# Performance work log

Measured on AMD Instinct MI355X. Metric: run time of the kernel, lower is better.

## Reference

```python
import jax, jax.numpy as jnp
import numpy as np

B, T, N, DIN, DR, DH, K = 8, 40, 1024, 16, 64, 64, 3
DT = 0.05
N_EULER = 2  # Euler sub-steps per observation interval (time_points per step)


def dconv(A, x, W, b):
    feats = [x]
    h = x
    for _ in range(K - 1):
        h = jnp.einsum('bnm,bmd->bnd', A, h)
        feats.append(h)
    return jnp.concatenate(feats, -1) @ W + b


def dcgru(x, h, A, Wg, bg, Wc, bc):
    g = jax.nn.sigmoid(dconv(A, jnp.concatenate([x, h], -1), Wg, bg))
    r, u = jnp.split(g, 2, -1)
    c = jnp.tanh(dconv(A, jnp.concatenate([x, r * h], -1), Wc, bc))
    return u * h + (1.0 - u) * c


def ode_f(h, A, W0, b0, Wout, bout):
    return jnp.tanh(jnp.tanh(dconv(A, h, W0, b0)) @ Wout + bout)


def setup_inputs() -> dict:
    key = jax.random.key(0)
    ks = jax.random.split(key, 32)
    p = lambda k, s: 0.1 * jax.random.normal(k, s, dtype=jnp.float32)
    values = jax.random.normal(ks[0], (B, T, N, DIN), dtype=jnp.float32)
    masks = (jax.random.uniform(ks[1], (B, T, N, DIN)) > 0.3).astype(jnp.float32)
    u = jax.random.uniform(ks[2], (B, N, N), dtype=jnp.float32)
    A = u / u.sum(-1, keepdims=True)  # row-normalized dense diffusion matrix
    d = dict(values=values, masks=masks, A=A,
             h0=p(ks[3], (1, 1, DR)) * 0.1, z0=p(ks[4], (1, 1, DR)) * 0.1,
             gV_Wg=p(ks[5], ((DIN + DR) * K, 2 * DR)), gV_bg=jnp.zeros((2 * DR,)),
             gV_Wc=p(ks[6], ((DIN + DR) * K, DR)), gV_bc=jnp.zeros((DR,)),
             gG_Wg=p(ks[7], ((DIN + DR) * K, 2 * DR)), gG_bg=jnp.zeros((2 * DR,)),
             gG_Wc=p(ks[8], ((DIN + DR) * K, DR)), gG_bc=jnp.zeros((DR,)),
             oV_W0=p(ks[9], (DR * K, DH)), oV_b0=jnp.zeros((DH,)),
             oV_Wout=p(ks[10], (DH, DR)), oV_bout=jnp.zeros((DR,)),
             oG_W0=p(ks[11], (DR * K, DH)), oG_b0=jnp.zeros((DH,)),
             oG_Wout=p(ks[12], (DH, DR)), oG_bout=jnp.zeros((DR,)),
             Wz1=p(ks[13], (DR, DR)), bz1=jnp.zeros((DR,)),
             Wz2=p(ks[14], (DR, DR)), bz2=jnp.zeros((DR,)),
             Wz3=p(ks[15], (DR, DR)), bz3=jnp.zeros((DR,)),
             Wo=p(ks[16], (DR, DIN)), bo=jnp.zeros((DIN,)))
    return d


def reference(values, masks, A, h0, z0,
              gV_Wg, gV_bg, gV_Wc, gV_bc, gG_Wg, gG_bg, gG_Wc, gG_bc,
              oV_W0, oV_b0, oV_Wout, oV_bout, oG_W0, oG_b0, oG_Wout, oG_bout,
              Wz1, bz1, Wz2, bz2, Wz3, bz3, Wo, bo):
    X = values * masks  # [B,T,N,DIN]
    obs = (jnp.abs(masks).sum(-1, keepdims=True) > 1e-4).astype(values.dtype)  # [B,T,N,1]
    hv = jnp.broadcast_to(h0, (B, N, DR))
    zv = jnp.broadcast_to(z0, (B, N, DR))
    dt = DT / N_EULER

    def step(carry, inp):
        hv, zv = carry
        x, m = inp  # [B,N,DIN], [B,N,1]
        for _ in range(N_EULER):  # Euler ODE integration over the interval
            hv = hv + dt * ode_f(hv, A, oV_W0, oV_b0, oV_Wout, oV_bout)
            zv = zv + dt * ode_f(zv, A, oG_W0, oG_b0, oG_Wout, oG_bout)
        hv1, zv1 = hv, zv
        hv2 = dcgru(x, hv1, A, gV_Wg, gV_bg, gV_Wc, gV_bc)
        zv2 = dcgru(x, zv1, A, gG_Wg, gG_bg, gG_Wc, gG_bc)
        hv_new = hv1 * (1.0 - m) + hv2 * m
        zv_new = zv1 * (1.0 - m) + zv2 * m
        return (hv_new, zv_new), (hv1, zv1, hv_new)

    xs = (jnp.swapaxes(X, 0, 1), jnp.swapaxes(obs, 0, 1))  # time-major
    _, (hv_pre, zv_pre, hv_post) = jax.lax.scan(step, (hv, zv), xs)
    hv_pre = jnp.swapaxes(hv_pre, 0, 1)   # [B,T,N,DR]
    zv_pre = jnp.swapaxes(zv_pre, 0, 1)
    gate = jax.nn.sigmoid(jnp.tanh(jnp.tanh(zv_pre @ Wz1 + bz1) @ Wz2 + bz2) @ Wz3 + bz3)
    X_pred = (hv_pre * gate) @ Wo + bo
    return X_pred[:, 1:, :, :]
```

## Files before the change

### kernel.cpp

```cpp
#include <hip/hip_runtime.h>
#include <math.h>


#define T_ 40

typedef __attribute__((ext_vector_type(8))) short short8;
typedef __attribute__((ext_vector_type(4))) float f32x4;

__device__ __forceinline__ float sigm(float x) { return 1.0f / (1.0f + expf(-x)); }

__device__ __forceinline__ unsigned short bfrnd(float x) {
  union { float f; unsigned int u; } v; v.f = x;
  unsigned int u = v.u + 0x7fffu + ((v.u >> 16) & 1u);
  return (unsigned short)(u >> 16);
}
__device__ __forceinline__ unsigned int pk2(float a, float b) {
  return (unsigned int)bfrnd(a) | ((unsigned int)bfrnd(b) << 16);
}

__global__ __launch_bounds__(256) void k_init(float* __restrict__ S, unsigned short* __restrict__ SB,
                                              const float* __restrict__ h0,
                                              const float* __restrict__ z0) {
  int idx = blockIdx.x * 256 + threadIdx.x;
  int c = idx & 63;
  S[idx] = (idx < (8192 * 64)) ? h0[c] : z0[c];
  int cc = (idx >> 10) & 63;
  float v2 = ((idx >> 16) < 8) ? h0[cc] : z0[cc];
  SB[idx] = bfrnd(v2);
}

__global__ __launch_bounds__(256) void k_asA(const float* __restrict__ A, unsigned short* __restrict__ AS) {
  size_t j = ((size_t)blockIdx.x * 256 + threadIdx.x) * 8;
  if (j >= (size_t)8 * 1024 * 1024) return;
  int b = (int)(j >> 20);
  size_t rem = j & 1048575;
  int r = (int)(rem >> 10), k = (int)(rem & 1023);
  const float* src = A + ((size_t)b << 20) + (size_t)r * 1024 + k;
  float4 v0 = *(const float4*)src;
  float4 v1 = *(const float4*)(src + 4);
  uint4 o;
  o.x = pk2(v0.x, v0.y); o.y = pk2(v0.z, v0.w);
  o.z = pk2(v1.x, v1.y); o.w = pk2(v1.z, v1.w);
  *(uint4*)(AS + ((size_t)b * 2048 + r) * 1024 + k) = o;
}

__global__ __launch_bounds__(256) void k_xb(const float* __restrict__ values,
                                            const float* __restrict__ masks,
                                            unsigned short* __restrict__ XB) {
  const int bt = blockIdx.x;
  const int n0 = blockIdx.y * 256;
  __shared__ float Ls[256][17];
  const int tid = threadIdx.x;
  size_t base = ((size_t)bt * 1024 + n0 + tid) * 16;
#pragma unroll
  for (int c4 = 0; c4 < 4; ++c4) {
    float4 v = *(const float4*)&values[base + c4 * 4];
    float4 m = *(const float4*)&masks[base + c4 * 4];
    Ls[tid][c4 * 4 + 0] = v.x * m.x; Ls[tid][c4 * 4 + 1] = v.y * m.y;
    Ls[tid][c4 * 4 + 2] = v.z * m.z; Ls[tid][c4 * 4 + 3] = v.w * m.w;
  }
  __syncthreads();
  const int c = tid >> 4, seg = tid & 15;
  uint4 o1, o2;
  o1.x = pk2(Ls[seg * 16 + 0][c], Ls[seg * 16 + 1][c]);
  o1.y = pk2(Ls[seg * 16 + 2][c], Ls[seg * 16 + 3][c]);
  o1.z = pk2(Ls[seg * 16 + 4][c], Ls[seg * 16 + 5][c]);
  o1.w = pk2(Ls[seg * 16 + 6][c], Ls[seg * 16 + 7][c]);
  o2.x = pk2(Ls[seg * 16 + 8][c], Ls[seg * 16 + 9][c]);
  o2.y = pk2(Ls[seg * 16 + 10][c], Ls[seg * 16 + 11][c]);
  o2.z = pk2(Ls[seg * 16 + 12][c], Ls[seg * 16 + 13][c]);
  o2.w = pk2(Ls[seg * 16 + 14][c], Ls[seg * 16 + 15][c]);
  unsigned short* dst = XB + ((size_t)bt * 16 + c) * 1024 + n0 + seg * 16;
  *(uint4*)dst = o1;
  *(uint4*)(dst + 8) = o2;
}

__global__ __launch_bounds__(256) void k_a2(const float* __restrict__ A, unsigned short* __restrict__ AS) {
  const int b = blockIdx.z;
  const int m0 = blockIdx.y * 128, n0 = blockIdx.x * 128;
  const float* Ab = A + ((size_t)b << 20);
  __shared__ float As[8][136];
  __shared__ float Bs[8][136];
  const int tx = threadIdx.x & 15, ty = threadIdx.x >> 4;
  float acc[8][8];
#pragma unroll
  for (int m = 0; m < 8; ++m)
#pragma unroll
    for (int n = 0; n < 8; ++n) acc[m][n] = 0.0f;

  for (int k0 = 0; k0 < 1024; k0 += 8) {
    int mm = threadIdx.x >> 1, k4 = (threadIdx.x & 1) * 4;
    float4 va = *(const float4*)&Ab[(size_t)(m0 + mm) * 1024 + k0 + k4];
    As[k4 + 0][mm] = va.x; As[k4 + 1][mm] = va.y; As[k4 + 2][mm] = va.z; As[k4 + 3][mm] = va.w;
    int kk = threadIdx.x >> 5, nn = (threadIdx.x & 31) * 4;
    float4 vb = *(const float4*)&Ab[(size_t)(k0 + kk) * 1024 + n0 + nn];
    *(float4*)&Bs[kk][nn] = vb;
    __syncthreads();
#pragma unroll
    for (int k = 0; k < 8; ++k) {
      float a[8], bb[8];
      *(float4*)&a[0] = *(float4*)&As[k][ty * 8];
      *(float4*)&a[4] = *(float4*)&As[k][ty * 8 + 4];
      *(float4*)&bb[0] = *(float4*)&Bs[k][tx * 8];
      *(float4*)&bb[4] = *(float4*)&Bs[k][tx * 8 + 4];
#pragma unroll
      for (int m = 0; m < 8; ++m)
#pragma unroll
        for (int n = 0; n < 8; ++n) acc[m][n] += a[m] * bb[n];
    }
    __syncthreads();
  }
#pragma unroll
  for (int m = 0; m < 8; ++m) {
    unsigned short* C = AS + ((size_t)b * 2048 + 1024 + m0 + ty * 8 + m) * 1024 + n0 + tx * 8;
    uint4 o;
    o.x = pk2(acc[m][0], acc[m][1]); o.y = pk2(acc[m][2], acc[m][3]);
    o.z = pk2(acc[m][4], acc[m][5]); o.w = pk2(acc[m][6], acc[m][7]);
    *(uint4*)C = o;
  }
}

template <int MODE>
__global__ __launch_bounds__(256) void k_fused(
    const unsigned short* __restrict__ AS,
    const unsigned short* __restrict__ XB,
    const unsigned short* __restrict__ SBr,
    unsigned short* __restrict__ SBw,
    const unsigned short* __restrict__ RHBin,
    unsigned short* __restrict__ RHBout,
    float* __restrict__ S, float* __restrict__ RH, float* __restrict__ U,
    const float* __restrict__ values, const float* __restrict__ masks,
    const float* __restrict__ W1h, const float* __restrict__ b1h,
    const float* __restrict__ W2h, const float* __restrict__ b2h,
    const float* __restrict__ W1z, const float* __restrict__ b1z,
    const float* __restrict__ W2z, const float* __restrict__ b2z,
    int t) {
  constexpr int NT = (MODE == 0) ? 8 : 9;
  constexpr int KF = (MODE == 0) ? 192 : 240;
  constexpr int FW = KF + 1;
  constexpr int NTILE = 2 + NT;
  constexpr int CHK = (MODE == 0) ? 64 : 48;
  constexpr int CW = (MODE == 1) ? 128 : 64;
  constexpr int CWP = CW + 4;
  constexpr int NCHK = KF / CHK;
  constexpr int R0_STAGE = 2 * NTILE * 1024;
  constexpr int R0_W = CHK * CWP * 4 + ((MODE == 0) ? 16 * 68 * 4 : 0);
  constexpr int R0 = (R0_STAGE > R0_W) ? R0_STAGE : R0_W;

  __shared__ __align__(16) char r0[R0];
  __shared__ float feats[2][16][FW];
  __shared__ float Ts[2][64][17];
  __shared__ float Ms[16];

  unsigned short* stg = (unsigned short*)r0;
  float* Wcs = (float*)r0;
  float* T1 = (float*)(r0 + 64 * 68 * 4);

  const int tid = threadIdx.x;
  const int w = tid >> 6, l = tid & 63;
  const int lr = l & 15, lk = l >> 4;
  const int b = blockIdx.y;
  const int n0 = blockIdx.x * 16;

  const unsigned short* ag =
      AS + ((size_t)b * 2048 + (w == 1 ? 1024 : 0) + n0 + lr) * 1024 + lk * 8;

  auto tsrc = [&](int ct) -> const unsigned short* {
    if (MODE == 0) {
      int st = ct >> 2, cl = ct & 3;
      return SBr + ((size_t)(st * 8 + b) * 64 + cl * 16 + lr) * 1024 + lk * 8;
    } else {
      if (ct == 0) return XB + ((size_t)(b * T_ + t) * 16 + lr) * 1024 + lk * 8;
      const unsigned short* base = (MODE == 1) ? SBr : RHBin;
      int st = (ct <= 4) ? 0 : 1;
      int cl = (ct <= 4) ? (ct - 1) : (ct - 5);
      return base + ((size_t)(st * 8 + b) * 64 + cl * 16 + lr) * 1024 + lk * 8;
    }
  };
  const unsigned short* bs0 = tsrc(w);
  const unsigned short* bs1 = tsrc(w + 4);
  const unsigned short* bs2 = (NT == 9 && w == 0) ? tsrc(8) : bs0;
  const int bcnt = (NT == 9 && w == 0) ? 3 : 2;

  if (MODE == 0) {
    for (int idx = tid; idx < 512; idx += 256) {
      int st = idx >> 8, rr = (idx >> 4) & 15, c4 = idx & 15;
      float4 v = *(const float4*)&S[((size_t)(st * 8 + b) * 1024 + n0 + rr) * 64 + c4 * 4];
      feats[st][rr][c4 * 4 + 0] = v.x; feats[st][rr][c4 * 4 + 1] = v.y;
      feats[st][rr][c4 * 4 + 2] = v.z; feats[st][rr][c4 * 4 + 3] = v.w;
    }
  } else {
    for (int idx = tid; idx < 64; idx += 256) {
      int rr = idx >> 2, c4 = idx & 3;
      size_t xo = ((size_t)(b * T_ + t) * 1024 + n0 + rr) * 16 + c4 * 4;
      float4 v = *(const float4*)&values[xo];
      float4 m = *(const float4*)&masks[xo];
      float xv[4] = {v.x * m.x, v.y * m.y, v.z * m.z, v.w * m.w};
#pragma unroll
      for (int j = 0; j < 4; ++j) {
        feats[0][rr][c4 * 4 + j] = xv[j];
        feats[1][rr][c4 * 4 + j] = xv[j];
      }
    }
    const float* bp = (MODE == 1) ? S : RH;
    for (int idx = tid; idx < 512; idx += 256) {
      int st = idx >> 8, rr = (idx >> 4) & 15, c4 = idx & 15;
      float4 v = *(const float4*)&bp[((size_t)(st * 8 + b) * 1024 + n0 + rr) * 64 + c4 * 4];
      feats[st][rr][16 + c4 * 4 + 0] = v.x; feats[st][rr][16 + c4 * 4 + 1] = v.y;
      feats[st][rr][16 + c4 * 4 + 2] = v.z; feats[st][rr][16 + c4 * 4 + 3] = v.w;
    }
  }
  if (MODE == 2 && tid < 16) {
    int n = n0 + tid;
    size_t xo = ((size_t)(b * T_ + t) * 1024 + n) * 16;
    float s = 0.0f;
    for (int d = 0; d < 16; ++d) s += fabsf(masks[xo + d]);
    Ms[tid] = (s > 1e-4f) ? 1.0f : 0.0f;
  }

  f32x4 acc[2][3];
#pragma unroll
  for (int rt = 0; rt < 2; ++rt)
#pragma unroll
    for (int ci = 0; ci < 3; ++ci) acc[rt][ci] = (f32x4){0.f, 0.f, 0.f, 0.f};

#define GLD(SRC, SLOT, BUF)                                                                   \
  __builtin_amdgcn_global_load_lds(                                                           \
      (const __attribute__((address_space(1))) void*)(SRC),                                   \
      (__attribute__((address_space(3))) void*)(stg + ((BUF)*NTILE + (SLOT)) * 512), 16, 0, 0)

#define STAGE(BUF, K0)                                                                        \
  {                                                                                           \
    if (w < 2) GLD(ag + (K0), w, BUF);                                                        \
    GLD(bs0 + (K0), 2 + w, BUF);                                                              \
    GLD(bs1 + (K0), 2 + w + 4, BUF);                                                          \
    if (NT == 9 && w == 0) GLD(bs2 + (K0), 2 + 8, BUF);                                       \
  }

  int cur = 0;
  STAGE(0, 0)
  __syncthreads();
  for (int step = 0; step < 32; ++step) {
    const int nxt = cur ^ 1;
    if (step < 31) STAGE(nxt, (step + 1) * 32)
    short8 a0f = *(const short8*)&stg[(cur * NTILE + 0) * 512 + l * 8];
    short8 a1f = *(const short8*)&stg[(cur * NTILE + 1) * 512 + l * 8];
    short8 b0f = *(const short8*)&stg[(cur * NTILE + 2 + w) * 512 + l * 8];
    short8 b1f = *(const short8*)&stg[(cur * NTILE + 2 + w + 4) * 512 + l * 8];
    acc[0][0] = __builtin_amdgcn_mfma_f32_16x16x32_bf16(a0f, b0f, acc[0][0], 0, 0, 0);
    acc[1][0] = __builtin_amdgcn_mfma_f32_16x16x32_bf16(a1f, b0f, acc[1][0], 0, 0, 0);
    acc[0][1] = __builtin_amdgcn_mfma_f32_16x16x32_bf16(a0f, b1f, acc[0][1], 0, 0, 0);
    acc[1][1] = __builtin_amdgcn_mfma_f32_16x16x32_bf16(a1f, b1f, acc[1][1], 0, 0, 0);
    if (NT == 9 && w == 0) {
      short8 b2f = *(const short8*)&stg[(cur * NTILE + 2 + 8) * 512 + l * 8];
      acc[0][2] = __builtin_amdgcn_mfma_f32_16x16x32_bf16(a0f, b2f, acc[0][2], 0, 0, 0);
      acc[1][2] = __builtin_amdgcn_mfma_f32_16x16x32_bf16(a1f, b2f, acc[1][2], 0, 0, 0);
    }
    __syncthreads();
    cur = nxt;
  }
#undef STAGE
#undef GLD

#pragma unroll
  for (int ci = 0; ci < 3; ++ci) {
    if (ci < bcnt) {
      const int ct = w + ci * 4;
#pragma unroll
      for (int rt = 0; rt < 2; ++rt) {
#pragma unroll
        for (int j = 0; j < 4; ++j) {
          float v = acc[rt][ci][j];
          int row = lk * 4 + j;
          if (MODE == 0) {
            int st = ct >> 2;
            feats[st][row][64 + rt * 64 + (ct & 3) * 16 + lr] = v;
          } else {
            if (ct == 0) {
              int col = 80 + rt * 80 + lr;
              feats[0][row][col] = v;
              feats[1][row][col] = v;
            } else {
              int st = (ct <= 4) ? 0 : 1;
              int cl = (ct <= 4) ? (ct - 1) : (ct - 5);
              feats[st][row][80 + rt * 80 + 16 + cl * 16 + lr] = v;
            }
          }
        }
      }
    }
  }
  __syncthreads();

  const int r_ = tid >> 4, cq = tid & 15;

  if (MODE == 0) {
    for (int st = 0; st < 2; ++st) {
      const float* W1 = st ? W1z : W1h;
      const float* B1 = st ? b1z : b1h;
      const float* W2 = st ? W2z : W2h;
      const float* B2 = st ? b2z : b2h;
      float a4[4] = {0, 0, 0, 0};
      for (int kc = 0; kc < NCHK; ++kc) {
        __syncthreads();
        for (int idx = tid; idx < 1024; idx += 256) {
          int k = idx >> 4, c4 = idx & 15;
          *(float4*)&Wcs[k * 68 + c4 * 4] = *(const float4*)&W1[(size_t)(kc * 64 + k) * 64 + c4 * 4];
        }
        __syncthreads();
#pragma unroll 8
        for (int k = 0; k < 64; ++k) {
          float f = feats[st][r_][kc * 64 + k];
          float4 w4 = *(float4*)&Wcs[k * 68 + cq * 4];
          a4[0] += f * w4.x; a4[1] += f * w4.y; a4[2] += f * w4.z; a4[3] += f * w4.w;
        }
      }
#pragma unroll
      for (int j = 0; j < 4; ++j) T1[r_ * 68 + cq * 4 + j] = tanhf(a4[j] + B1[cq * 4 + j]);
      __syncthreads();
      for (int idx = tid; idx < 1024; idx += 256) {
        int k = idx >> 4, c4 = idx & 15;
        *(float4*)&Wcs[k * 68 + c4 * 4] = *(const float4*)&W2[(size_t)k * 64 + c4 * 4];
      }
      __syncthreads();
      float o4[4] = {0, 0, 0, 0};
#pragma unroll 8
      for (int k = 0; k < 64; ++k) {
        float f = T1[r_ * 68 + k];
        float4 w4 = *(float4*)&Wcs[k * 68 + cq * 4];
        o4[0] += f * w4.x; o4[1] += f * w4.y; o4[2] += f * w4.z; o4[3] += f * w4.w;
      }
      size_t g = ((size_t)(st * 8 + b) * 1024 + n0 + r_) * 64 + cq * 4;
#pragma unroll
      for (int j = 0; j < 4; ++j) {
        float ns = S[g + j] + 0.025f * tanhf(o4[j] + B2[cq * 4 + j]);
        S[g + j] = ns;
        Ts[st][cq * 4 + j][r_] = ns;
      }
      __syncthreads();
    }
  } else if (MODE == 1) {
    for (int st = 0; st < 2; ++st) {
      const float* W1 = st ? W1z : W1h;
      const float* B1 = st ? b1z : b1h;
      float a8[8] = {0, 0, 0, 0, 0, 0, 0, 0};
      for (int kc = 0; kc < NCHK; ++kc) {
        __syncthreads();
        for (int idx = tid; idx < 1536; idx += 256) {
          int k = idx >> 5, c4 = idx & 31;
          *(float4*)&Wcs[k * 132 + c4 * 4] = *(const float4*)&W1[(size_t)(kc * 48 + k) * 128 + c4 * 4];
        }
        __syncthreads();
#pragma unroll 8
        for (int k = 0; k < 48; ++k) {
          float f = feats[st][r_][kc * 48 + k];
          float4 wA = *(float4*)&Wcs[k * 132 + cq * 8];
          float4 wB = *(float4*)&Wcs[k * 132 + cq * 8 + 4];
          a8[0] += f * wA.x; a8[1] += f * wA.y; a8[2] += f * wA.z; a8[3] += f * wA.w;
          a8[4] += f * wB.x; a8[5] += f * wB.y; a8[6] += f * wB.z; a8[7] += f * wB.w;
        }
      }
      size_t g = ((size_t)(st * 8 + b) * 1024 + n0 + r_) * 64;
      if (cq < 8) {
#pragma unroll
        for (int j = 0; j < 8; ++j) {
          int c = cq * 8 + j;
          float rr = sigm(a8[j] + B1[c]);
          float rhv = rr * feats[st][r_][16 + c];
          RH[g + c] = rhv;
          Ts[st][c][r_] = rhv;
        }
      } else {
#pragma unroll
        for (int j = 0; j < 8; ++j) {
          int c = (cq - 8) * 8 + j;
          U[g + c] = sigm(a8[j] + B1[64 + c]);
        }
      }
      __syncthreads();
    }
  } else {
    for (int st = 0; st < 2; ++st) {
      const float* W1 = st ? W1z : W1h;
      const float* B1 = st ? b1z : b1h;
      float a4[4] = {0, 0, 0, 0};
      for (int kc = 0; kc < NCHK; ++kc) {
        __syncthreads();
        for (int idx = tid; idx < 768; idx += 256) {
          int k = idx >> 4, c4 = idx & 15;
          *(float4*)&Wcs[k * 68 + c4 * 4] = *(const float4*)&W1[(size_t)(kc * 48 + k) * 64 + c4 * 4];
        }
        __syncthreads();
#pragma unroll 8
        for (int k = 0; k < 48; ++k) {
          float f = feats[st][r_][kc * 48 + k];
          float4 w4 = *(float4*)&Wcs[k * 68 + cq * 4];
          a4[0] += f * w4.x; a4[1] += f * w4.y; a4[2] += f * w4.z; a4[3] += f * w4.w;
        }
      }
      size_t g = ((size_t)(st * 8 + b) * 1024 + n0 + r_) * 64;
      float m = Ms[r_];
#pragma unroll
      for (int j = 0; j < 4; ++j) {
        int c = cq * 4 + j;
        float cc = tanhf(a4[j] + B1[c]);
        float h1 = S[g + c];
        float u = U[g + c];
        float h2 = u * h1 + (1.0f - u) * cc;
        float ns = h1 * (1.0f - m) + h2 * m;
        S[g + c] = ns;
        Ts[st][c][r_] = ns;
      }
      __syncthreads();
    }
  }

  {
    unsigned short* dstbuf = (MODE == 1) ? RHBout : SBw;
    int st = tid >> 7, c = (tid >> 1) & 63, p = tid & 1;
    float* tp = &Ts[st][c][p * 8];
    uint4 o;
    o.x = pk2(tp[0], tp[1]); o.y = pk2(tp[2], tp[3]);
    o.z = pk2(tp[4], tp[5]); o.w = pk2(tp[6], tp[7]);
    *(uint4*)(dstbuf + ((size_t)(st * 8 + b) * 64 + c) * 1024 + n0 + p * 8) = o;
  }
}

__global__ __launch_bounds__(256) void k_out(const float* __restrict__ S,
    const float* __restrict__ Wz1, const float* __restrict__ bz1,
    const float* __restrict__ Wz2, const float* __restrict__ bz2,
    const float* __restrict__ Wz3, const float* __restrict__ bz3,
    const float* __restrict__ Wo, const float* __restrict__ bo,
    float* __restrict__ out, int t) {
  __shared__ float Zs[32][68];
  __shared__ float T1s[32][68];
  __shared__ float Hs[32][68];
  __shared__ float Wc[64][64];
  __shared__ float bias[64];
  const int rowbase = blockIdx.x * 32;
  const int r = threadIdx.x >> 3, q = threadIdx.x & 7;

  for (int idx = threadIdx.x; idx < 2048; idx += 256) {
    int rr = idx >> 6, c = idx & 63;
    size_t g = (size_t)(rowbase + rr);
    Zs[rr][c] = S[(size_t)524288 + g * 64 + c];
    Hs[rr][c] = S[g * 64 + c];
  }

#define LAYER(SRC, DST, WPTR, BPTR, ACT)                                            \
  __syncthreads();                                                                  \
  for (int idx = threadIdx.x; idx < 1024; idx += 256)                               \
    ((float4*)Wc)[idx] = ((const float4*)(WPTR))[idx];                              \
  if (threadIdx.x < 64) bias[threadIdx.x] = (BPTR)[threadIdx.x];                    \
  __syncthreads();                                                                  \
  {                                                                                 \
    float ac[8] = {0, 0, 0, 0, 0, 0, 0, 0};                                         \
    _Pragma("unroll 8") for (int k = 0; k < 64; ++k) {                              \
      float f = SRC[r][k];                                                          \
      float4 w0 = *(float4*)&Wc[k][q * 8];                                          \
      float4 w1 = *(float4*)&Wc[k][q * 8 + 4];                                      \
      ac[0] += f * w0.x; ac[1] += f * w0.y; ac[2] += f * w0.z; ac[3] += f * w0.w;   \
      ac[4] += f * w1.x; ac[5] += f * w1.y; ac[6] += f * w1.z; ac[7] += f * w1.w;   \
    }                                                                               \
    _Pragma("unroll") for (int j = 0; j < 8; ++j)                                   \
        DST[r][q * 8 + j] = ACT(ac[j] + bias[q * 8 + j]);                           \
  }

  LAYER(Zs, T1s, Wz1, bz1, tanhf)
  LAYER(T1s, Zs, Wz2, bz2, tanhf)
  LAYER(Zs, T1s, Wz3, bz3, sigm)
#undef LAYER

  __syncthreads();
  for (int idx = threadIdx.x; idx < 256; idx += 256)
    ((float4*)Wc)[idx] = ((const float4*)Wo)[idx];
  if (threadIdx.x < 16) bias[threadIdx.x] = bo[threadIdx.x];
  __syncthreads();

  const float* WcF = &Wc[0][0];
  float a0 = 0.0f, a1 = 0.0f;
#pragma unroll 8
  for (int k = 0; k < 64; ++k) {
    float f = Hs[r][k] * T1s[r][k];
    a0 += f * WcF[k * 16 + q * 2];
    a1 += f * WcF[k * 16 + q * 2 + 1];
  }
  size_t g = (size_t)(rowbase + r);
  int b = (int)(g >> 10), n = (int)(g & 1023);
  size_t o = (((size_t)b * 39 + (t - 1)) * 1024 + n) * 16 + q * 2;
  out[o]     = a0 + bias[q * 2];
  out[o + 1] = a1 + bias[q * 2 + 1];
}

extern "C" void kernel_launch(void* const* d_in, const int* in_sizes, int n_in,
                              void* d_out, int out_size, void* d_ws, size_t ws_size,
                              hipStream_t stream) {
  const float* values = (const float*)d_in[0];
  const float* masks  = (const float*)d_in[1];
  const float* A      = (const float*)d_in[2];
  const float* h0     = (const float*)d_in[3];
  const float* z0     = (const float*)d_in[4];
  const float* gV_Wg  = (const float*)d_in[5];
  const float* gV_bg  = (const float*)d_in[6];
  const float* gV_Wc  = (const float*)d_in[7];
  const float* gV_bc  = (const float*)d_in[8];
  const float* gG_Wg  = (const float*)d_in[9];
  const float* gG_bg  = (const float*)d_in[10];
  const float* gG_Wc  = (const float*)d_in[11];
  const float* gG_bc  = (const float*)d_in[12];
  const float* oV_W0  = (const float*)d_in[13];
  const float* oV_b0  = (const float*)d_in[14];
  const float* oV_Wout = (const float*)d_in[15];
  const float* oV_bout = (const float*)d_in[16];
  const float* oG_W0  = (const float*)d_in[17];
  const float* oG_b0  = (const float*)d_in[18];
  const float* oG_Wout = (const float*)d_in[19];
  const float* oG_bout = (const float*)d_in[20];
  const float* Wz1 = (const float*)d_in[21];
  const float* bz1 = (const float*)d_in[22];
  const float* Wz2 = (const float*)d_in[23];
  const float* bz2 = (const float*)d_in[24];
  const float* Wz3 = (const float*)d_in[25];
  const float* bz3 = (const float*)d_in[26];
  const float* Wo  = (const float*)d_in[27];
  const float* bo  = (const float*)d_in[28];
  float* out = (float*)d_out;

  if (ws_size < (size_t)62914560) return;
  char* ws = (char*)d_ws;
  float* S            = (float*)(ws + 0);
  float* RH           = (float*)(ws + 4194304);
  float* U            = (float*)(ws + 8388608);
  unsigned short* SBa = (unsigned short*)(ws + 12582912);
  unsigned short* SBb = (unsigned short*)(ws + 14680064);
  unsigned short* RHB = (unsigned short*)(ws + 16777216);
  unsigned short* XB  = (unsigned short*)(ws + 18874368);
  unsigned short* AS  = (unsigned short*)(ws + 29360128);

  k_asA<<<4096, 256, 0, stream>>>(A, AS);
  k_a2<<<dim3(8, 8, 8), 256, 0, stream>>>(A, AS);
  k_init<<<4096, 256, 0, stream>>>(S, SBa, h0, z0);
  k_xb<<<dim3(320, 4), 256, 0, stream>>>(values, masks, XB);

  const dim3 fg(64, 8);
  for (int t = 0; t < T_; ++t) {
    k_fused<0><<<fg, 256, 0, stream>>>(AS, XB, SBa, SBb, RHB, RHB, S, RH, U, values, masks,
                                       oV_W0, oV_b0, oV_Wout, oV_bout,
                                       oG_W0, oG_b0, oG_Wout, oG_bout, t);
    k_fused<0><<<fg, 256, 0, stream>>>(AS, XB, SBb, SBa, RHB, RHB, S, RH, U, values, masks,
                                       oV_W0, oV_b0, oV_Wout, oV_bout,
                                       oG_W0, oG_b0, oG_Wout, oG_bout, t);
    if (t >= 1)
      k_out<<<256, 256, 0, stream>>>(S, Wz1, bz1, Wz2, bz2, Wz3, bz3, Wo, bo, out, t);
    if (t < T_ - 1) {
      k_fused<1><<<fg, 256, 0, stream>>>(AS, XB, SBa, SBb, RHB, RHB, S, RH, U, values, masks,
                                         gV_Wg, gV_bg, nullptr, nullptr,
                                         gG_Wg, gG_bg, nullptr, nullptr, t);
      k_fused<2><<<fg, 256, 0, stream>>>(AS, XB, SBa, SBa, RHB, RHB, S, RH, U, values, masks,
                                         gV_Wc, gV_bc, nullptr, nullptr,
                                         gG_Wc, gG_bc, nullptr, nullptr, t);
    }
  }
}
```

Before: 8.997 ms.

## Fuse output head into ODE kernel, MFMA A^2 precompute, remap block grid

```diff
diff --git a/kernel.cpp b/kernel.cpp
--- a/kernel.cpp
+++ b/kernel.cpp
@@ -42,6 +42,84 @@
   o.x = pk2(v0.x, v0.y); o.y = pk2(v0.z, v0.w);
   o.z = pk2(v1.x, v1.y); o.w = pk2(v1.z, v1.w);
   *(uint4*)(AS + ((size_t)b * 2048 + r) * 1024 + k) = o;
+}
+
+__global__ __launch_bounds__(256) void k_tr(const float* __restrict__ A, unsigned short* __restrict__ ATB) {
+  const int b = blockIdx.z, k0 = blockIdx.y * 64, n0 = blockIdx.x * 64;
+  __shared__ float Ls[64][65];
+  const float* Ab = A + ((size_t)b << 20);
+  for (int idx = threadIdx.x; idx < 1024; idx += 256) {
+    int kr = idx >> 4, cg = idx & 15;
+    float4 v = *(const float4*)&Ab[(size_t)(k0 + kr) * 1024 + n0 + cg * 4];
+    Ls[kr][cg * 4 + 0] = v.x; Ls[kr][cg * 4 + 1] = v.y;
+    Ls[kr][cg * 4 + 2] = v.z; Ls[kr][cg * 4 + 3] = v.w;
+  }
+  __syncthreads();
+  const int nr = threadIdx.x >> 2, seg = threadIdx.x & 3;
+  const int ks = seg * 16;
+  uint4 o1, o2;
+  o1.x = pk2(Ls[ks + 0][nr], Ls[ks + 1][nr]);
+  o1.y = pk2(Ls[ks + 2][nr], Ls[ks + 3][nr]);
+  o1.z = pk2(Ls[ks + 4][nr], Ls[ks + 5][nr]);
+  o1.w = pk2(Ls[ks + 6][nr], Ls[ks + 7][nr]);
+  o2.x = pk2(Ls[ks + 8][nr], Ls[ks + 9][nr]);
+  o2.y = pk2(Ls[ks + 10][nr], Ls[ks + 11][nr]);
+  o2.z = pk2(Ls[ks + 12][nr], Ls[ks + 13][nr]);
+  o2.w = pk2(Ls[ks + 14][nr], Ls[ks + 15][nr]);
+  unsigned short* dst = ATB + ((size_t)b * 1024 + n0 + nr) * 1024 + k0 + ks;
+  *(uint4*)dst = o1;
+  *(uint4*)(dst + 8) = o2;
+}
+
+__global__ __launch_bounds__(256) void k_a2m(unsigned short* __restrict__ AS,
+                                             const unsigned short* __restrict__ ATB) {
+  __shared__ __align__(16) unsigned short stg[2][12][512];
+  const int tid = threadIdx.x;
+  const int w = tid >> 6, l = tid & 63;
+  const int lr = l & 15, lk = l >> 4;
+  const int b = blockIdx.z, m0 = blockIdx.y * 64, n0 = blockIdx.x * 128;
+
+  const unsigned short* ag  = AS  + ((size_t)b * 2048 + m0 + w * 16 + lr) * 1024 + lk * 8;
+  const unsigned short* bg0 = ATB + ((size_t)b * 1024 + n0 + w * 16 + lr) * 1024 + lk * 8;
+  const unsigned short* bg1 = ATB + ((size_t)b * 1024 + n0 + (w + 4) * 16 + lr) * 1024 + lk * 8;
+
+  f32x4 acc[8];
+#pragma unroll
+  for (int ct = 0; ct < 8; ++ct) acc[ct] = (f32x4){0.f, 0.f, 0.f, 0.f};
+
+#define GLD2(SRC, SLOT, BUF)                                                                  \
+  __builtin_amdgcn_global_load_lds(                                                          \
+      (const __attribute__((address_space(1))) void*)(SRC),                                   \
+      (__attribute__((address_space(3))) void*)(&stg[BUF][SLOT][0]), 16, 0, 0)
+
+  int cur = 0;
+  GLD2(ag, w, 0); GLD2(bg0, 4 + w, 0); GLD2(bg1, 8 + w, 0);
+  __syncthreads();
+  for (int step = 0; step < 32; ++step) {
+    const int nxt = cur ^ 1;
+    if (step < 31) {
+      const int K0 = (step + 1) * 32;
+      GLD2(ag + K0, w, nxt); GLD2(bg0 + K0, 4 + w, nxt); GLD2(bg1 + K0, 8 + w, nxt);
+    }
+    short8 af = *(const short8*)&stg[cur][w][l * 8];
+#pragma unroll
+    for (int ct = 0; ct < 8; ++ct) {
+      short8 bf = *(const short8*)&stg[cur][4 + ct][l * 8];
+      acc[ct] = __builtin_amdgcn_mfma_f32_16x16x32_bf16(af, bf, acc[ct], 0, 0, 0);
+    }
+    __syncthreads();
+    cur = nxt;
+  }
+#undef GLD2
+
+#pragma unroll
+  for (int ct = 0; ct < 8; ++ct) {
+#pragma unroll
+    for (int j = 0; j < 4; ++j) {
+      AS[((size_t)b * 2048 + 1024 + m0 + w * 16 + lk * 4 + j) * 1024 + n0 + ct * 16 + lr] =
+          bfrnd(acc[ct][j]);
+    }
+  }
 }
 
 __global__ __launch_bounds__(256) void k_xb(const float* __restrict__ values,
@@ -75,52 +153,7 @@
   *(uint4*)(dst + 8) = o2;
 }
 
-__global__ __launch_bounds__(256) void k_a2(const float* __restrict__ A, unsigned short* __restrict__ AS) {
-  const int b = blockIdx.z;
-  const int m0 = blockIdx.y * 128, n0 = blockIdx.x * 128;
-  const float* Ab = A + ((size_t)b << 20);
-  __shared__ float As[8][136];
-  __shared__ float Bs[8][136];
-  const int tx = threadIdx.x & 15, ty = threadIdx.x >> 4;
-  float acc[8][8];
-#pragma unroll
-  for (int m = 0; m < 8; ++m)
-#pragma unroll
-    for (int n = 0; n < 8; ++n) acc[m][n] = 0.0f;
-
-  for (int k0 = 0; k0 < 1024; k0 += 8) {
-    int mm = threadIdx.x >> 1, k4 = (threadIdx.x & 1) * 4;
-    float4 va = *(const float4*)&Ab[(size_t)(m0 + mm) * 1024 + k0 + k4];
-    As[k4 + 0][mm] = va.x; As[k4 + 1][mm] = va.y; As[k4 + 2][mm] = va.z; As[k4 + 3][mm] = va.w;
-    int kk = threadIdx.x >> 5, nn = (threadIdx.x & 31) * 4;
-    float4 vb = *(const float4*)&Ab[(size_t)(k0 + kk) * 1024 + n0 + nn];
-    *(float4*)&Bs[kk][nn] = vb;
-    __syncthreads();
-#pragma unroll
-    for (int k = 0; k < 8; ++k) {
-      float a[8], bb[8];
-      *(float4*)&a[0] = *(float4*)&As[k][ty * 8];
-      *(float4*)&a[4] = *(float4*)&As[k][ty * 8 + 4];
-      *(float4*)&bb[0] = *(float4*)&Bs[k][tx * 8];
-      *(float4*)&bb[4] = *(float4*)&Bs[k][tx * 8 + 4];
-#pragma unroll
-      for (int m = 0; m < 8; ++m)
-#pragma unroll
-        for (int n = 0; n < 8; ++n) acc[m][n] += a[m] * bb[n];
-    }
-    __syncthreads();
-  }
-#pragma unroll
-  for (int m = 0; m < 8; ++m) {
-    unsigned short* C = AS + ((size_t)b * 2048 + 1024 + m0 + ty * 8 + m) * 1024 + n0 + tx * 8;
-    uint4 o;
-    o.x = pk2(acc[m][0], acc[m][1]); o.y = pk2(acc[m][2], acc[m][3]);
-    o.z = pk2(acc[m][4], acc[m][5]); o.w = pk2(acc[m][6], acc[m][7]);
-    *(uint4*)C = o;
-  }
-}
-
-template <int MODE>
+template <int MODE, int OUT>
 __global__ __launch_bounds__(256) void k_fused(
     const unsigned short* __restrict__ AS,
     const unsigned short* __restrict__ XB,
@@ -134,7 +167,11 @@
     const float* __restrict__ W2h, const float* __restrict__ b2h,
     const float* __restrict__ W1z, const float* __restrict__ b1z,
     const float* __restrict__ W2z, const float* __restrict__ b2z,
-    int t) {
+    const float* __restrict__ Wz1, const float* __restrict__ bz1,
+    const float* __restrict__ Wz2, const float* __restrict__ bz2,
+    const float* __restrict__ Wz3, const float* __restrict__ bz3,
+    const float* __restrict__ Wo, const float* __restrict__ bo,
+    float* __restrict__ outp, int t) {
   constexpr int NT = (MODE == 0) ? 8 : 9;
   constexpr int KF = (MODE == 0) ? 192 : 240;
   constexpr int FW = KF + 1;
@@ -151,6 +188,7 @@
   __shared__ float feats[2][16][FW];
   __shared__ float Ts[2][64][17];
   __shared__ float Ms[16];
+  __shared__ float gb[64];
 
   unsigned short* stg = (unsigned short*)r0;
   float* Wcs = (float*)r0;
@@ -159,8 +197,8 @@
   const int tid = threadIdx.x;
   const int w = tid >> 6, l = tid & 63;
   const int lr = l & 15, lk = l >> 4;
-  const int b = blockIdx.y;
-  const int n0 = blockIdx.x * 16;
+  const int b = blockIdx.x & 7;
+  const int n0 = (blockIdx.x >> 3) * 16;
 
   const unsigned short* ag =
       AS + ((size_t)b * 2048 + (w == 1 ? 1024 : 0) + n0 + lr) * 1024 + lk * 8;
@@ -424,72 +462,43 @@
     o.z = pk2(tp[4], tp[5]); o.w = pk2(tp[6], tp[7]);
     *(uint4*)(dstbuf + ((size_t)(st * 8 + b) * 64 + c) * 1024 + n0 + p * 8) = o;
   }
-}
-
-__global__ __launch_bounds__(256) void k_out(const float* __restrict__ S,
-    const float* __restrict__ Wz1, const float* __restrict__ bz1,
-    const float* __restrict__ Wz2, const float* __restrict__ bz2,
-    const float* __restrict__ Wz3, const float* __restrict__ bz3,
-    const float* __restrict__ Wo, const float* __restrict__ bo,
-    float* __restrict__ out, int t) {
-  __shared__ float Zs[32][68];
-  __shared__ float T1s[32][68];
-  __shared__ float Hs[32][68];
-  __shared__ float Wc[64][64];
-  __shared__ float bias[64];
-  const int rowbase = blockIdx.x * 32;
-  const int r = threadIdx.x >> 3, q = threadIdx.x & 7;
-
-  for (int idx = threadIdx.x; idx < 2048; idx += 256) {
-    int rr = idx >> 6, c = idx & 63;
-    size_t g = (size_t)(rowbase + rr);
-    Zs[rr][c] = S[(size_t)524288 + g * 64 + c];
-    Hs[rr][c] = S[g * 64 + c];
-  }
-
-#define LAYER(SRC, DST, WPTR, BPTR, ACT)                                            \
-  __syncthreads();                                                                  \
-  for (int idx = threadIdx.x; idx < 1024; idx += 256)                               \
-    ((float4*)Wc)[idx] = ((const float4*)(WPTR))[idx];                              \
-  if (threadIdx.x < 64) bias[threadIdx.x] = (BPTR)[threadIdx.x];                    \
-  __syncthreads();                                                                  \
-  {                                                                                 \
-    float ac[8] = {0, 0, 0, 0, 0, 0, 0, 0};                                         \
-    _Pragma("unroll 8") for (int k = 0; k < 64; ++k) {                              \
-      float f = SRC[r][k];                                                          \
-      float4 w0 = *(float4*)&Wc[k][q * 8];                                          \
-      float4 w1 = *(float4*)&Wc[k][q * 8 + 4];                                      \
-      ac[0] += f * w0.x; ac[1] += f * w0.y; ac[2] += f * w0.z; ac[3] += f * w0.w;   \
-      ac[4] += f * w1.x; ac[5] += f * w1.y; ac[6] += f * w1.z; ac[7] += f * w1.w;   \
-    }                                                                               \
-    _Pragma("unroll") for (int j = 0; j < 8; ++j)                                   \
-        DST[r][q * 8 + j] = ACT(ac[j] + bias[q * 8 + j]);                           \
-  }
-
-  LAYER(Zs, T1s, Wz1, bz1, tanhf)
-  LAYER(T1s, Zs, Wz2, bz2, tanhf)
-  LAYER(Zs, T1s, Wz3, bz3, sigm)
-#undef LAYER
-
-  __syncthreads();
-  for (int idx = threadIdx.x; idx < 256; idx += 256)
-    ((float4*)Wc)[idx] = ((const float4*)Wo)[idx];
-  if (threadIdx.x < 16) bias[threadIdx.x] = bo[threadIdx.x];
-  __syncthreads();
-
-  const float* WcF = &Wc[0][0];
-  float a0 = 0.0f, a1 = 0.0f;
+
+  if constexpr (MODE == 0 && OUT) {
+#define OLAYER(SRCEXPR, DSTOFF, WPTR, BPTR, ACT)                                     \
+    __syncthreads();                                                                 \
+    for (int idx = tid; idx < 1024; idx += 256) {                                    \
+      int k = idx >> 4, c4 = idx & 15;                                               \
+      *(float4*)&Wcs[k * 68 + c4 * 4] = *(const float4*)&(WPTR)[(size_t)k * 64 + c4 * 4]; \
+    }                                                                                \
+    if (tid < 64) gb[tid] = (BPTR)[tid];                                             \
+    __syncthreads();                                                                 \
+    {                                                                                \
+      float a4[4] = {0, 0, 0, 0};                                                    \
+      _Pragma("unroll 8") for (int k = 0; k < 64; ++k) {                             \
+        float f = (SRCEXPR);                                                         \
+        float4 w4 = *(float4*)&Wcs[k * 68 + cq * 4];                                 \
+        a4[0] += f * w4.x; a4[1] += f * w4.y; a4[2] += f * w4.z; a4[3] += f * w4.w;  \
+      }                                                                              \
+      _Pragma("unroll") for (int j = 0; j < 4; ++j)                                  \
+          feats[0][r_][(DSTOFF) + cq * 4 + j] = ACT(a4[j] + gb[cq * 4 + j]);         \
+    }
+
+    OLAYER(Ts[1][k][r_],           96, Wz1, bz1, tanhf)
+    OLAYER(feats[0][r_][96 + k],    0, Wz2, bz2, tanhf)
+    OLAYER(feats[0][r_][k],        96, Wz3, bz3, sigm)
+#undef OLAYER
+    __syncthreads();
+    for (int idx = tid; idx < 256; idx += 256)
+      ((float4*)Wcs)[idx] = ((const float4*)Wo)[idx];
+    if (tid < 16) gb[tid] = bo[tid];
+    __syncthreads();
+    float a0 = 0.0f;
 #pragma unroll 8
-  for (int k = 0; k < 64; ++k) {
-    float f = Hs[r][k] * T1s[r][k];
-    a0 += f * WcF[k * 16 + q * 2];
-    a1 += f * WcF[k * 16 + q * 2 + 1];
-  }
-  size_t g = (size_t)(rowbase + r);
-  int b = (int)(g >> 10), n = (int)(g & 1023);
-  size_t o = (((size_t)b * 39 + (t - 1)) * 1024 + n) * 16 + q * 2;
-  out[o]     = a0 + bias[q * 2];
-  out[o + 1] = a1 + bias[q * 2 + 1];
+    for (int k = 0; k < 64; ++k)
+      a0 += Ts[0][k][r_] * feats[0][r_][96 + k] * Wcs[k * 16 + cq];
+    size_t o = (((size_t)b * 39 + (t - 1)) * 1024 + n0 + r_) * 16 + cq;
+    outp[o] = a0 + gb[cq];
+  }
 }
 
 extern "C" void kernel_launch(void* const* d_in, const int* in_sizes, int n_in,
@@ -526,7 +535,7 @@
   const float* bo  = (const float*)d_in[28];
   float* out = (float*)d_out;
 
-  if (ws_size < (size_t)62914560) return;
+  if (ws_size < (size_t)79691776) return;
   char* ws = (char*)d_ws;
   float* S            = (float*)(ws + 0);
   float* RH           = (float*)(ws + 4194304);
@@ -536,29 +545,38 @@
   unsigned short* RHB = (unsigned short*)(ws + 16777216);
   unsigned short* XB  = (unsigned short*)(ws + 18874368);
   unsigned short* AS  = (unsigned short*)(ws + 29360128);
+  unsigned short* ATB = (unsigned short*)(ws + 62914560);
 
   k_asA<<<4096, 256, 0, stream>>>(A, AS);
-  k_a2<<<dim3(8, 8, 8), 256, 0, stream>>>(A, AS);
+  k_tr<<<dim3(16, 16, 8), 256, 0, stream>>>(A, ATB);
+  k_a2m<<<dim3(8, 16, 8), 256, 0, stream>>>(AS, ATB);
   k_init<<<4096, 256, 0, stream>>>(S, SBa, h0, z0);
   k_xb<<<dim3(320, 4), 256, 0, stream>>>(values, masks, XB);
 
-  const dim3 fg(64, 8);
   for (int t = 0; t < T_; ++t) {
-    k_fused<0><<<fg, 256, 0, stream>>>(AS, XB, SBa, SBb, RHB, RHB, S, RH, U, values, masks,
-                                       oV_W0, oV_b0, oV_Wout, oV_bout,
-                                       oG_W0, oG_b0, oG_Wout, oG_bout, t);
-    k_fused<0><<<fg, 256, 0, stream>>>(AS, XB, SBb, SBa, RHB, RHB, S, RH, U, values, masks,
-                                       oV_W0, oV_b0, oV_Wout, oV_bout,
-                                       oG_W0, oG_b0, oG_Wout, oG_bout, t);
-    if (t >= 1)
-      k_out<<<256, 256, 0, stream>>>(S, Wz1, bz1, Wz2, bz2, Wz3, bz3, Wo, bo, out, t);
+    k_fused<0, 0><<<512, 256, 0, stream>>>(AS, XB, SBa, SBb, RHB, RHB, S, RH, U, values, masks,
+                                           oV_W0, oV_b0, oV_Wout, oV_bout,
+                                           oG_W0, oG_b0, oG_Wout, oG_bout,
+                                           Wz1, bz1, Wz2, bz2, Wz3, bz3, Wo, bo, out, t);
+    if (t == 0)
+      k_fused<0, 0><<<512, 256, 0, stream>>>(AS, XB, SBb, SBa, RHB, RHB, S, RH, U, values, masks,
+                                             oV_W0, oV_b0, oV_Wout, oV_bout,
+                                             oG_W0, oG_b0, oG_Wout, oG_bout,
+                                             Wz1, bz1, Wz2, bz2, Wz3, bz3, Wo, bo, out, t);
+    else
+      k_fused<0, 1><<<512, 256, 0, stream>>>(AS, XB, SBb, SBa, RHB, RHB, S, RH, U, values, masks,
+                                             oV_W0, oV_b0, oV_Wout, oV_bout,
+                                             oG_W0, oG_b0, oG_Wout, oG_bout,
+                                             Wz1, bz1, Wz2, bz2, Wz3, bz3, Wo, bo, out, t);
     if (t < T_ - 1) {
-      k_fused<1><<<fg, 256, 0, stream>>>(AS, XB, SBa, SBb, RHB, RHB, S, RH, U, values, masks,
-                                         gV_Wg, gV_bg, nullptr, nullptr,
-                                         gG_Wg, gG_bg, nullptr, nullptr, t);
-      k_fused<2><<<fg, 256, 0, stream>>>(AS, XB, SBa, SBa, RHB, RHB, S, RH, U, values, masks,
-                                         gV_Wc, gV_bc, nullptr, nullptr,
-                                         gG_Wc, gG_bc, nullptr, nullptr, t);
-    }
-  }
-}
+      k_fused<1, 0><<<512, 256, 0, stream>>>(AS, XB, SBa, SBb, RHB, RHB, S, RH, U, values, masks,
+                                             gV_Wg, gV_bg, nullptr, nullptr,
+                                             gG_Wg, gG_bg, nullptr, nullptr,
+                                             Wz1, bz1, Wz2, bz2, Wz3, bz3, Wo, bo, out, t);
+      k_fused<2, 0><<<512, 256, 0, stream>>>(AS, XB, SBa, SBa, RHB, RHB, S, RH, U, values, masks,
+                                             gV_Wc, gV_bc, nullptr, nullptr,
+                                             gG_Wc, gG_bc, nullptr, nullptr,
+                                             Wz1, bz1, Wz2, bz2, Wz3, bz3, Wo, bo, out, t);
+    }
+  }
+}
```

After: 8.564 ms. 1.05x faster.
